# Optimization experiments

Measured on AMD Instinct MI355X. Metric: run time of the kernel, lower is better.

The kernel has to match this reference:

```python
import jax, jax.numpy as jnp
import numpy as np

B, T, TWO_H = 64, 512, 1024  # batch, prev decoding steps, 2*hidden_dim


def setup_inputs() -> dict:
    key = jax.random.key(0)
    k1, k2, k3 = jax.random.split(key, 3)
    h_d_t = jax.random.normal(k1, (B, TWO_H), dtype=jnp.float32)
    prev_h_dec = jax.random.normal(k2, (B, T, TWO_H), dtype=jnp.float32)
    # nn.Bilinear(2H, 2H, attn_dim=1) weight, trunc_norm_init_std ~ 1e-4 typical
    W = jax.random.normal(k3, (1, TWO_H, TWO_H), dtype=jnp.float32) * 1e-4
    return {"h_d_t": h_d_t, "prev_h_dec": prev_h_dec, "W": W}


def reference(h_d_t, prev_h_dec, W):
    # Bilinear score: s[b,t] = h_d_t[b] @ W[0] @ prev_h_dec[b,t]
    q = jnp.einsum('bd,de->be', h_d_t, W[0])          # (B, 2H) -- one small GEMM
    attn_score = jnp.einsum('be,bte->bt', q, prev_h_dec)  # (B, T)
    alpha_t = jax.nn.softmax(attn_score, axis=1)      # (B, T)
    ct_d = jnp.einsum('bt,btd->bd', alpha_t, prev_h_dec)  # (B, 2H)
    new_prev = jnp.concatenate([prev_h_dec, h_d_t[:, None, :]], axis=1)  # (B, T+1, 2H)
    return (ct_d, new_prev)
```

## Files before the change

kernel.cpp:

```cpp
#include <hip/hip_runtime.h>
#include <math.h>

#define BB    64
#define TT    512
#define TWOH  1024
#define WPB   4
#define TCB   WPB
#define NCHUNK (TT / TCB)
#define NP_STRIDE ((TT + 1) * TWOH)

typedef float vfloat4 __attribute__((ext_vector_type(4)));


__device__ __forceinline__ void gload_lds16(const float* g, float* l) {
    __builtin_amdgcn_global_load_lds(
        (const __attribute__((address_space(1))) unsigned int*)g,
        (__attribute__((address_space(3))) unsigned int*)l,
        16, 0, 0);
}

__global__ __launch_bounds__(256) void k_qgemm(const float* __restrict__ h,
                                               const float* __restrict__ W,
                                               float* __restrict__ q) {
    const int tid = threadIdx.x;
    const int e   = blockIdx.x * 256 + tid;
    const int b   = blockIdx.y;

    __shared__ float sh[TWOH];
    ((vfloat4*)sh)[tid] = ((const vfloat4*)(h + (size_t)b * TWOH))[tid];
    __syncthreads();

    const float* __restrict__ Wp = W + e;
    float acc = 0.f;
    #pragma unroll 16
    for (int d = 0; d < TWOH; ++d)
        acc = fmaf(sh[d], Wp[(size_t)d * TWOH], acc);

    q[(size_t)b * TWOH + e] = acc;
}

__global__ __launch_bounds__(256, 8) void k_scores_ct(const float* __restrict__ prev,
                                                      const float* __restrict__ q,
                                                      float* __restrict__ ws_m,
                                                      float* __restrict__ ws_l,
                                                      float* __restrict__ ws_ct) {
    const int tid  = threadIdx.x;
    const int lane = tid & 63;
    const int wid  = tid >> 6;
    const int c    = blockIdx.x;
    const int b    = blockIdx.y;
    const int t    = c * TCB + wid;

    __shared__ float srow[WPB][TWOH];
    __shared__ float sscore[WPB];

    const float* gbase = prev + ((size_t)b * TT + t) * TWOH;
    #pragma unroll
    for (int j = 0; j < 4; ++j)
        gload_lds16(gbase + j * 256 + lane * 4, &srow[wid][j * 256]);

    const vfloat4* __restrict__ qv = (const vfloat4*)(q + (size_t)b * TWOH);
    const vfloat4 q0 = qv[lane];
    const vfloat4 q1 = qv[64 + lane];
    const vfloat4 q2 = qv[128 + lane];
    const vfloat4 q3 = qv[192 + lane];

    asm volatile("s_waitcnt vmcnt(0)" ::: "memory");
    __builtin_amdgcn_sched_barrier(0);

    const vfloat4* sr = (const vfloat4*)&srow[wid][0];
    const vfloat4 v0 = sr[lane];
    const vfloat4 v1 = sr[64 + lane];
    const vfloat4 v2 = sr[128 + lane];
    const vfloat4 v3 = sr[192 + lane];
    float d0 = v0.x * q0.x; d0 = fmaf(v0.y, q0.y, d0);
    d0 = fmaf(v0.z, q0.z, d0); d0 = fmaf(v0.w, q0.w, d0);
    float d1 = v1.x * q1.x; d1 = fmaf(v1.y, q1.y, d1);
    d1 = fmaf(v1.z, q1.z, d1); d1 = fmaf(v1.w, q1.w, d1);
    float d2 = v2.x * q2.x; d2 = fmaf(v2.y, q2.y, d2);
    d2 = fmaf(v2.z, q2.z, d2); d2 = fmaf(v2.w, q2.w, d2);
    float d3 = v3.x * q3.x; d3 = fmaf(v3.y, q3.y, d3);
    d3 = fmaf(v3.z, q3.z, d3); d3 = fmaf(v3.w, q3.w, d3);
    float pd = (d0 + d1) + (d2 + d3);
    #pragma unroll
    for (int off = 32; off > 0; off >>= 1)
        pd += __shfl_xor(pd, off, 64);
    if (lane == 0) sscore[wid] = pd;
    __syncthreads();

    const float s0 = sscore[0], s1 = sscore[1], s2 = sscore[2], s3 = sscore[3];
    const float M  = fmaxf(fmaxf(s0, s1), fmaxf(s2, s3));
    const float a0 = __expf(s0 - M);
    const float a1 = __expf(s1 - M);
    const float a2 = __expf(s2 - M);
    const float a3 = __expf(s3 - M);
    const float L  = (a0 + a1) + (a2 + a3);

    const vfloat4 x0 = ((const vfloat4*)&srow[0][0])[tid];
    const vfloat4 x1 = ((const vfloat4*)&srow[1][0])[tid];
    const vfloat4 x2 = ((const vfloat4*)&srow[2][0])[tid];
    const vfloat4 x3 = ((const vfloat4*)&srow[3][0])[tid];
    vfloat4 o;
    o.x = fmaf(a3, x3.x, fmaf(a2, x2.x, fmaf(a1, x1.x, a0 * x0.x)));
    o.y = fmaf(a3, x3.y, fmaf(a2, x2.y, fmaf(a1, x1.y, a0 * x0.y)));
    o.z = fmaf(a3, x3.z, fmaf(a2, x2.z, fmaf(a1, x1.z, a0 * x0.z)));
    o.w = fmaf(a3, x3.w, fmaf(a2, x2.w, fmaf(a1, x1.w, a0 * x0.w)));
    ((vfloat4*)(ws_ct + ((size_t)b * NCHUNK + c) * TWOH))[tid] = o;
    if (tid == 0) {
        ws_m[b * NCHUNK + c] = M;
        ws_l[b * NCHUNK + c] = L;
    }
}

__global__ __launch_bounds__(256) void k_finalize(const float* __restrict__ h,
                                                  const float* __restrict__ ws_m,
                                                  const float* __restrict__ ws_l,
                                                  const float* __restrict__ ws_ct,
                                                  float* __restrict__ out_ct,
                                                  float* __restrict__ out_np) {
    const int tid = threadIdx.x;
    const int e   = blockIdx.x * 256 + tid;
    const int b   = blockIdx.y;

    const float* __restrict__ wm = ws_m + b * NCHUNK;
    const float* __restrict__ wl = ws_l + b * NCHUNK;

    float M = -INFINITY;
    #pragma unroll 32
    for (int i = 0; i < NCHUNK; ++i) M = fmaxf(M, wm[i]);

    const float* __restrict__ cp = ws_ct + (size_t)b * NCHUNK * TWOH + e;
    float L = 0.f;
    float acc = 0.f;
    #pragma unroll 32
    for (int i = 0; i < NCHUNK; ++i) {
        const float ce = __expf(wm[i] - M);
        L   = fmaf(ce, wl[i], L);
        acc = fmaf(ce, cp[(size_t)i * TWOH], acc);
    }
    out_ct[b * TWOH + e] = acc * (1.0f / L);

    out_np[(size_t)b * NP_STRIDE + (size_t)TT * TWOH + e] = h[b * TWOH + e];
}

extern "C" void kernel_launch(void* const* d_in, const int* in_sizes, int n_in,
                              void* d_out, int out_size, void* d_ws, size_t ws_size,
                              hipStream_t stream) {
    const float* h    = (const float*)d_in[0];
    const float* prev = (const float*)d_in[1];
    const float* W    = (const float*)d_in[2];
    float* out    = (float*)d_out;
    float* out_ct = out;
    float* out_np = out + BB * TWOH;

    float* q   = (float*)d_ws;
    float* wsm = q + BB * TWOH;
    float* wsl = wsm + BB * NCHUNK;
    float* wsc = wsl + BB * NCHUNK;

    k_qgemm    <<<dim3(4, BB),      256, 0, stream>>>(h, W, q);
    k_scores_ct<<<dim3(NCHUNK, BB), 256, 0, stream>>>(prev, q, wsm, wsl, wsc);

    hipMemcpy2DAsync(out_np, (size_t)NP_STRIDE * sizeof(float),
                     prev,   (size_t)TT * TWOH * sizeof(float),
                     (size_t)TT * TWOH * sizeof(float), BB,
                     hipMemcpyDeviceToDevice, stream);

    k_finalize <<<dim3(4, BB),      256, 0, stream>>>(h, wsm, wsl, wsc, out_ct, out_np);
}
```

Baseline: 325.6 us.

## Fuse prev_h_dec copy into score kernel and split accumulators in GEMV/finalize

The separate 2D device memcpy that builds new_prev is removed. Each score wave now writes its staged row of prev_h_dec straight to the output, so the 128 MB input is read once instead of twice. The q GEMV and the finalize reduction also switch to four independent accumulators to shorten FMA dependency chains. The fused stores add write traffic to the score kernel and may slow its memory pipeline.

```diff
diff --git a/kernel.cpp b/kernel.cpp
--- a/kernel.cpp
+++ b/kernel.cpp
@@ -31,16 +31,20 @@
     __syncthreads();
 
     const float* __restrict__ Wp = W + e;
-    float acc = 0.f;
-    #pragma unroll 16
-    for (int d = 0; d < TWOH; ++d)
-        acc = fmaf(sh[d], Wp[(size_t)d * TWOH], acc);
-
-    q[(size_t)b * TWOH + e] = acc;
+    float a0 = 0.f, a1 = 0.f, a2 = 0.f, a3 = 0.f;
+    #pragma unroll 8
+    for (int d = 0; d < TWOH; d += 4) {
+        a0 = fmaf(sh[d],     Wp[(size_t)(d)     * TWOH], a0);
+        a1 = fmaf(sh[d + 1], Wp[(size_t)(d + 1) * TWOH], a1);
+        a2 = fmaf(sh[d + 2], Wp[(size_t)(d + 2) * TWOH], a2);
+        a3 = fmaf(sh[d + 3], Wp[(size_t)(d + 3) * TWOH], a3);
+    }
+    q[(size_t)b * TWOH + e] = (a0 + a1) + (a2 + a3);
 }
 
 __global__ __launch_bounds__(256, 8) void k_scores_ct(const float* __restrict__ prev,
                                                       const float* __restrict__ q,
+                                                      float* __restrict__ out_np,
                                                       float* __restrict__ ws_m,
                                                       float* __restrict__ ws_l,
                                                       float* __restrict__ ws_ct) {
@@ -69,10 +73,16 @@
     __builtin_amdgcn_sched_barrier(0);
 
     const vfloat4* sr = (const vfloat4*)&srow[wid][0];
+    vfloat4* __restrict__ nprow =
+        (vfloat4*)(out_np + (size_t)b * NP_STRIDE + (size_t)t * TWOH) + lane;
     const vfloat4 v0 = sr[lane];
     const vfloat4 v1 = sr[64 + lane];
     const vfloat4 v2 = sr[128 + lane];
     const vfloat4 v3 = sr[192 + lane];
+    nprow[0]   = v0;
+    nprow[64]  = v1;
+    nprow[128] = v2;
+    nprow[192] = v3;
     float d0 = v0.x * q0.x; d0 = fmaf(v0.y, q0.y, d0);
     d0 = fmaf(v0.z, q0.z, d0); d0 = fmaf(v0.w, q0.w, d0);
     float d1 = v1.x * q1.x; d1 = fmaf(v1.y, q1.y, d1);
@@ -130,14 +140,25 @@
     for (int i = 0; i < NCHUNK; ++i) M = fmaxf(M, wm[i]);
 
     const float* __restrict__ cp = ws_ct + (size_t)b * NCHUNK * TWOH + e;
-    float L = 0.f;
-    float acc = 0.f;
-    #pragma unroll 32
-    for (int i = 0; i < NCHUNK; ++i) {
-        const float ce = __expf(wm[i] - M);
-        L   = fmaf(ce, wl[i], L);
-        acc = fmaf(ce, cp[(size_t)i * TWOH], acc);
+    float L0 = 0.f, L1 = 0.f, L2 = 0.f, L3 = 0.f;
+    float c0 = 0.f, c1 = 0.f, c2 = 0.f, c3 = 0.f;
+    #pragma unroll 8
+    for (int i = 0; i < NCHUNK; i += 4) {
+        const float e0 = __expf(wm[i]     - M);
+        const float e1 = __expf(wm[i + 1] - M);
+        const float e2 = __expf(wm[i + 2] - M);
+        const float e3 = __expf(wm[i + 3] - M);
+        L0 = fmaf(e0, wl[i],     L0);
+        L1 = fmaf(e1, wl[i + 1], L1);
+        L2 = fmaf(e2, wl[i + 2], L2);
+        L3 = fmaf(e3, wl[i + 3], L3);
+        c0 = fmaf(e0, cp[(size_t)(i)     * TWOH], c0);
+        c1 = fmaf(e1, cp[(size_t)(i + 1) * TWOH], c1);
+        c2 = fmaf(e2, cp[(size_t)(i + 2) * TWOH], c2);
+        c3 = fmaf(e3, cp[(size_t)(i + 3) * TWOH], c3);
     }
+    const float L   = (L0 + L1) + (L2 + L3);
+    const float acc = (c0 + c1) + (c2 + c3);
     out_ct[b * TWOH + e] = acc * (1.0f / L);
 
     out_np[(size_t)b * NP_STRIDE + (size_t)TT * TWOH + e] = h[b * TWOH + e];
@@ -159,12 +180,6 @@
     float* wsc = wsl + BB * NCHUNK;
 
     k_qgemm    <<<dim3(4, BB),      256, 0, stream>>>(h, W, q);
-    k_scores_ct<<<dim3(NCHUNK, BB), 256, 0, stream>>>(prev, q, wsm, wsl, wsc);
-
-    hipMemcpy2DAsync(out_np, (size_t)NP_STRIDE * sizeof(float),
-                     prev,   (size_t)TT * TWOH * sizeof(float),
-                     (size_t)TT * TWOH * sizeof(float), BB,
-                     hipMemcpyDeviceToDevice, stream);
-
+    k_scores_ct<<<dim3(NCHUNK, BB), 256, 0, stream>>>(prev, q, out_np, wsm, wsl, wsc);
     k_finalize <<<dim3(4, BB),      256, 0, stream>>>(h, wsm, wsl, wsc, out_ct, out_np);
 }
```

Measured after the change: 286.0 us. 1.14x faster.
